# Performance work log

Measured on AMD Instinct MI355X. Metric: run time of the kernel, lower is better.

The kernel has to match this reference:

```python
import jax, jax.numpy as jnp
import numpy as np

L = 16
IN0 = 7  # 3 + 3 + 1 per the torch module
CH = [16, 32, 16]
N = 500000
NEG_SLOPE = 0.2


def setup_inputs() -> dict:
    key = jax.random.key(0)
    ks = jax.random.split(key, 5)
    x = jax.random.normal(ks[0], (N, IN0), dtype=jnp.float32)
    idx = jax.random.randint(ks[1], (N,), 0, L, dtype=jnp.int32)
    # kaiming-uniform-like init scale per layer fan-in
    def init_w(k, shape):
        fan_in = shape[1]
        bound = float(np.sqrt(6.0 / fan_in))
        return jax.random.uniform(k, shape, dtype=jnp.float32, minval=-bound, maxval=bound)
    W0 = init_w(ks[2], (L, IN0, CH[0]))
    W1 = init_w(ks[3], (L, CH[0], CH[1]))
    W2 = init_w(ks[4], (L, CH[1], CH[2]))
    b0 = jnp.zeros((L, CH[0]), dtype=jnp.float32)
    b1 = jnp.zeros((L, CH[1]), dtype=jnp.float32)
    b2 = jnp.zeros((L, CH[2]), dtype=jnp.float32)
    return {"x": x, "idx": idx, "W0": W0, "b0": b0, "W1": W1, "b1": b1, "W2": W2, "b2": b2}


def reference(x, idx, W0, b0, W1, b1, W2, b2):
    # Per-point expert-indexed MLP: h <- LeakyReLU(h @ W[idx] + b[idx]) per layer.
    h = x
    for W, b in ((W0, b0), (W1, b1), (W2, b2)):
        # gather per-point weight [N, in, out] and bias [N, out], vec-mat per point
        h = jax.nn.leaky_relu(
            jnp.einsum("nc,nco->no", h, W[idx]) + b[idx],
            negative_slope=NEG_SLOPE,
        )
    return h
```

## Files before the change

kernel.cpp:

```cpp
#include <hip/hip_runtime.h>


#define L_EXP 16
#define IN0   7
#define C0    16
#define C1    32
#define C2    16
#define NEG   0.2f
#define BLK   256
#define MPT   4
#define SEGPAD (BLK * MPT)
#define CHUNK  1024
#define NBM    512

#define WS_PART  64
#define WS_STAGE 16384

__global__ void k_hist(const int* __restrict__ idx, int n, int* __restrict__ ws) {
    __shared__ int bins[L_EXP];
    int t = threadIdx.x;
    if (t < L_EXP) bins[t] = 0;
    __syncthreads();
#pragma unroll
    for (int s = 0; s < CHUNK / BLK; ++s) {
        int i = blockIdx.x * CHUNK + s * BLK + t;
        if (i < n) atomicAdd(&bins[idx[i] & 15], 1);
    }
    __syncthreads();
    if (t < L_EXP) ws[WS_PART + t * NBM + blockIdx.x] = bins[t];
}

__global__ void k_scan(int* __restrict__ ws, int nblk) {
    int t = threadIdx.x;
    int e = t >> 6, l = t & 63;
    int running = 0;
    for (int c = 0; c < nblk; c += 64) {
        int b = c + l;
        int v = (b < nblk) ? ws[WS_PART + e * NBM + b] : 0;
        int s = v;
#pragma unroll
        for (int d = 1; d < 64; d <<= 1) {
            int u = __shfl_up(s, d, 64);
            if (l >= d) s += u;
        }
        if (b < nblk) ws[WS_PART + e * NBM + b] = running + (s - v);
        running += __shfl(s, 63, 64);
    }
    if (l == 0) ws[e] = running;
    __syncthreads();
    if (t == 0) {
        int run = 0;
        for (int q = 0; q < L_EXP; ++q) {
            ws[16 + q] = run;
            run += ((ws[q] + SEGPAD - 1) / SEGPAD) * SEGPAD;
        }
        ws[32] = run;
    }
}

__global__ void k_scatter(const int* __restrict__ idx, const float* __restrict__ x,
                          int n, const int* __restrict__ ws, float* __restrict__ stage) {
    __shared__ int soff[L_EXP];
    __shared__ int lcount[L_EXP];
    int t = threadIdx.x;
    if (t < L_EXP) {
        soff[t] = ws[16 + t] + ws[WS_PART + t * NBM + blockIdx.x];
        lcount[t] = 0;
    }
    __syncthreads();
#pragma unroll
    for (int s = 0; s < CHUNK / BLK; ++s) {
        int i = blockIdx.x * CHUNK + s * BLK + t;
        if (i < n) {
            int e = idx[i] & 15;
            int r = atomicAdd(&lcount[e], 1);
            int pos = soff[e] + r;
            float xv[IN0];
#pragma unroll
            for (int c = 0; c < IN0; ++c) xv[c] = x[i * IN0 + c];
            float4* sp = reinterpret_cast<float4*>(stage + (size_t)pos * 8);
            sp[0] = make_float4(xv[0], xv[1], xv[2], xv[3]);
            sp[1] = make_float4(xv[4], xv[5], xv[6], __int_as_float(i));
        }
    }
}

__device__ __forceinline__ float leaky(float a) { return fmaxf(a, NEG * a); }

__device__ __forceinline__ float4 f4_fma(float s, float4 w, float4 a) {
    a.x = fmaf(s, w.x, a.x);
    a.y = fmaf(s, w.y, a.y);
    a.z = fmaf(s, w.z, a.z);
    a.w = fmaf(s, w.w, a.w);
    return a;
}

__global__ void __launch_bounds__(BLK, 2) k_mlp(
    const int* __restrict__ meta, const float* __restrict__ stage,
    const float* __restrict__ W0, const float* __restrict__ b0,
    const float* __restrict__ W1, const float* __restrict__ b1,
    const float* __restrict__ W2, const float* __restrict__ b2,
    float* __restrict__ out) {
    __shared__ __align__(16) float sW0[IN0 * C0];
    __shared__ __align__(16) float sB0[C0];
    __shared__ __align__(16) float sW1[C0 * C1];
    __shared__ __align__(16) float sB1[C1];
    __shared__ __align__(16) float sW2[C1 * C2];
    __shared__ __align__(16) float sB2[C2];

    int start = blockIdx.x * SEGPAD;
    if (start >= meta[32]) return;

    int e = 0;
    while (start >= meta[16 + e + 1]) ++e;
    e = __builtin_amdgcn_readfirstlane(e);

    int t = threadIdx.x;
    {
        const float* w0p = W0 + e * (IN0 * C0);
        const float* w1p = W1 + e * (C0 * C1);
        const float* w2p = W2 + e * (C1 * C2);
        if (t < IN0 * C0) sW0[t] = w0p[t];
        if (t >= 128 && t < 128 + C0) sB0[t - 128] = b0[e * C0 + (t - 128)];
        if (t >= 160 && t < 160 + C1) sB1[t - 160] = b1[e * C1 + (t - 160)];
        if (t >= 192 && t < 192 + C2) sB2[t - 192] = b2[e * C2 + (t - 192)];
        for (int k = t; k < C0 * C1; k += BLK) sW1[k] = w1p[k];
        for (int k = t; k < C1 * C2; k += BLK) sW2[k] = w2p[k];
    }
    __syncthreads();

    int seg = meta[16 + e];
    int cnt = meta[e];
    int j0 = start - seg + t;

    float xv[MPT][IN0];
    int   pid[MPT];
    bool  act[MPT];
#pragma unroll
    for (int m = 0; m < MPT; ++m) {
        int j = j0 + m * BLK;
        act[m] = (j < cnt);
        const float4* sp = reinterpret_cast<const float4*>(stage + (size_t)(seg + j) * 8);
        float4 a = sp[0];
        float4 b = sp[1];
        xv[m][0] = a.x; xv[m][1] = a.y; xv[m][2] = a.z; xv[m][3] = a.w;
        xv[m][4] = b.x; xv[m][5] = b.y; xv[m][6] = b.z;
        pid[m] = __float_as_int(b.w);
    }
    __builtin_amdgcn_sched_barrier(0);

    float h0[MPT][C0];
#pragma unroll
    for (int og = 0; og < C0 / 4; ++og) {
        float4 bb = *reinterpret_cast<const float4*>(&sB0[og * 4]);
        float4 acc[MPT];
#pragma unroll
        for (int m = 0; m < MPT; ++m) acc[m] = bb;
#pragma unroll
        for (int c = 0; c < IN0; ++c) {
            float4 w = *reinterpret_cast<const float4*>(&sW0[c * C0 + og * 4]);
#pragma unroll
            for (int m = 0; m < MPT; ++m) acc[m] = f4_fma(xv[m][c], w, acc[m]);
        }
#pragma unroll
        for (int m = 0; m < MPT; ++m) {
            h0[m][og * 4 + 0] = leaky(acc[m].x);
            h0[m][og * 4 + 1] = leaky(acc[m].y);
            h0[m][og * 4 + 2] = leaky(acc[m].z);
            h0[m][og * 4 + 3] = leaky(acc[m].w);
        }
        if (og == 1) __builtin_amdgcn_sched_barrier(0);
    }
    __builtin_amdgcn_sched_barrier(0);

    float4 h2[MPT][C2 / 4];
#pragma unroll
    for (int og = 0; og < C2 / 4; ++og) {
        float4 bb = *reinterpret_cast<const float4*>(&sB2[og * 4]);
#pragma unroll
        for (int m = 0; m < MPT; ++m) h2[m][og] = bb;
    }
#pragma unroll 1
    for (int ch = 0; ch < C1 / 4; ++ch) {
        float4 tv[MPT];
        float4 bb = *reinterpret_cast<const float4*>(&sB1[ch * 4]);
#pragma unroll
        for (int m = 0; m < MPT; ++m) tv[m] = bb;
#pragma unroll
        for (int c = 0; c < C0; ++c) {
            float4 w = *reinterpret_cast<const float4*>(&sW1[c * C1 + ch * 4]);
#pragma unroll
            for (int m = 0; m < MPT; ++m) tv[m] = f4_fma(h0[m][c], w, tv[m]);
        }
#pragma unroll
        for (int m = 0; m < MPT; ++m) {
            tv[m].x = leaky(tv[m].x); tv[m].y = leaky(tv[m].y);
            tv[m].z = leaky(tv[m].z); tv[m].w = leaky(tv[m].w);
        }
#pragma unroll
        for (int q = 0; q < 4; ++q) {
#pragma unroll
            for (int og = 0; og < C2 / 4; ++og) {
                float4 w = *reinterpret_cast<const float4*>(&sW2[(ch * 4 + q) * C2 + og * 4]);
#pragma unroll
                for (int m = 0; m < MPT; ++m) {
                    float s = (q == 0) ? tv[m].x : (q == 1) ? tv[m].y
                                       : (q == 2) ? tv[m].z : tv[m].w;
                    h2[m][og] = f4_fma(s, w, h2[m][og]);
                }
            }
        }
        __builtin_amdgcn_sched_barrier(0);
    }

#pragma unroll
    for (int m = 0; m < MPT; ++m) {
        if (act[m]) {
            float4* outp = reinterpret_cast<float4*>(out + (size_t)pid[m] * C2);
#pragma unroll
            for (int og = 0; og < C2 / 4; ++og) {
                float4 o = h2[m][og];
                o.x = leaky(o.x); o.y = leaky(o.y);
                o.z = leaky(o.z); o.w = leaky(o.w);
                outp[og] = o;
            }
        }
    }
}

extern "C" void kernel_launch(void* const* d_in, const int* in_sizes, int n_in,
                              void* d_out, int out_size, void* d_ws, size_t ws_size,
                              hipStream_t stream) {
    const float* x  = (const float*)d_in[0];
    const int*  idx = (const int*)d_in[1];
    const float* W0 = (const float*)d_in[2];
    const float* b0 = (const float*)d_in[3];
    const float* W1 = (const float*)d_in[4];
    const float* b1 = (const float*)d_in[5];
    const float* W2 = (const float*)d_in[6];
    const float* b2 = (const float*)d_in[7];
    float* out = (float*)d_out;

    int n = in_sizes[1];
    int* ws = (int*)d_ws;
    float* stage = (float*)d_ws + WS_STAGE;

    int nblk = (n + CHUNK - 1) / CHUNK;
    k_hist<<<nblk, BLK, 0, stream>>>(idx, n, ws);
    k_scan<<<1, 1024, 0, stream>>>(ws, nblk);
    k_scatter<<<nblk, BLK, 0, stream>>>(idx, x, n, ws, stage);

    int mblk = (n + L_EXP * (SEGPAD - 1) + SEGPAD - 1) / SEGPAD;
    k_mlp<<<mblk, BLK, 0, stream>>>(ws, stage, W0, b0, W1, b1, W2, b2, out);
}
```

Baseline: 120.9 us.

## Scatter point indices instead of staging inputs and gather inputs in MLP

```diff
diff --git a/kernel.cpp b/kernel.cpp
--- a/kernel.cpp
+++ b/kernel.cpp
@@ -14,17 +14,24 @@
 #define NBM    512
 
 #define WS_PART  64
-#define WS_STAGE 16384
+#define WS_PERM  16384
 
 __global__ void k_hist(const int* __restrict__ idx, int n, int* __restrict__ ws) {
     __shared__ int bins[L_EXP];
     int t = threadIdx.x;
     if (t < L_EXP) bins[t] = 0;
     __syncthreads();
-#pragma unroll
-    for (int s = 0; s < CHUNK / BLK; ++s) {
-        int i = blockIdx.x * CHUNK + s * BLK + t;
-        if (i < n) atomicAdd(&bins[idx[i] & 15], 1);
+    int i4 = blockIdx.x * CHUNK + t * 4;
+    if (i4 + 3 < n) {
+        int4 v = *reinterpret_cast<const int4*>(idx + i4);
+        atomicAdd(&bins[v.x & 15], 1);
+        atomicAdd(&bins[v.y & 15], 1);
+        atomicAdd(&bins[v.z & 15], 1);
+        atomicAdd(&bins[v.w & 15], 1);
+    } else {
+#pragma unroll
+        for (int q = 0; q < 4; ++q)
+            if (i4 + q < n) atomicAdd(&bins[idx[i4 + q] & 15], 1);
     }
     __syncthreads();
     if (t < L_EXP) ws[WS_PART + t * NBM + blockIdx.x] = bins[t];
@@ -58,8 +65,8 @@
     }
 }
 
-__global__ void k_scatter(const int* __restrict__ idx, const float* __restrict__ x,
-                          int n, const int* __restrict__ ws, float* __restrict__ stage) {
+__global__ void k_scatter(const int* __restrict__ idx, int n,
+                          int* __restrict__ ws) {
     __shared__ int soff[L_EXP];
     __shared__ int lcount[L_EXP];
     int t = threadIdx.x;
@@ -68,19 +75,14 @@
         lcount[t] = 0;
     }
     __syncthreads();
-#pragma unroll
-    for (int s = 0; s < CHUNK / BLK; ++s) {
-        int i = blockIdx.x * CHUNK + s * BLK + t;
+    int i4 = blockIdx.x * CHUNK + t * 4;
+#pragma unroll
+    for (int q = 0; q < 4; ++q) {
+        int i = i4 + q;
         if (i < n) {
             int e = idx[i] & 15;
             int r = atomicAdd(&lcount[e], 1);
-            int pos = soff[e] + r;
-            float xv[IN0];
-#pragma unroll
-            for (int c = 0; c < IN0; ++c) xv[c] = x[i * IN0 + c];
-            float4* sp = reinterpret_cast<float4*>(stage + (size_t)pos * 8);
-            sp[0] = make_float4(xv[0], xv[1], xv[2], xv[3]);
-            sp[1] = make_float4(xv[4], xv[5], xv[6], __int_as_float(i));
+            ws[WS_PERM + soff[e] + r] = i;
         }
     }
 }
@@ -96,7 +98,7 @@
 }
 
 __global__ void __launch_bounds__(BLK, 2) k_mlp(
-    const int* __restrict__ meta, const float* __restrict__ stage,
+    const int* __restrict__ meta, const float* __restrict__ x,
     const float* __restrict__ W0, const float* __restrict__ b0,
     const float* __restrict__ W1, const float* __restrict__ b1,
     const float* __restrict__ W2, const float* __restrict__ b2,
@@ -140,12 +142,13 @@
     for (int m = 0; m < MPT; ++m) {
         int j = j0 + m * BLK;
         act[m] = (j < cnt);
-        const float4* sp = reinterpret_cast<const float4*>(stage + (size_t)(seg + j) * 8);
-        float4 a = sp[0];
-        float4 b = sp[1];
+        int p = meta[WS_PERM + seg + j];
+        pid[m] = act[m] ? p : 0;
+        const float* xp = x + (size_t)pid[m] * IN0;
+        float4 a = *reinterpret_cast<const float4*>(xp);
+        float4 b = *reinterpret_cast<const float4*>(xp + 3);
         xv[m][0] = a.x; xv[m][1] = a.y; xv[m][2] = a.z; xv[m][3] = a.w;
-        xv[m][4] = b.x; xv[m][5] = b.y; xv[m][6] = b.z;
-        pid[m] = __float_as_int(b.w);
+        xv[m][4] = b.y; xv[m][5] = b.z; xv[m][6] = b.w;
     }
     __builtin_amdgcn_sched_barrier(0);
 
@@ -243,13 +246,12 @@
 
     int n = in_sizes[1];
     int* ws = (int*)d_ws;
-    float* stage = (float*)d_ws + WS_STAGE;
 
     int nblk = (n + CHUNK - 1) / CHUNK;
     k_hist<<<nblk, BLK, 0, stream>>>(idx, n, ws);
     k_scan<<<1, 1024, 0, stream>>>(ws, nblk);
-    k_scatter<<<nblk, BLK, 0, stream>>>(idx, x, n, ws, stage);
+    k_scatter<<<nblk, BLK, 0, stream>>>(idx, n, ws);
 
     int mblk = (n + L_EXP * (SEGPAD - 1) + SEGPAD - 1) / SEGPAD;
-    k_mlp<<<mblk, BLK, 0, stream>>>(ws, stage, W0, b0, W1, b1, W2, b2, out);
-}
+    k_mlp<<<mblk, BLK, 0, stream>>>(ws, x, W0, b0, W1, b1, W2, b2, out);
+}
```

Result: no change. 118.9 us (-1.7%).
